# Kernel optimization log

Measured on AMD Instinct MI355X. Metric: run time of the kernel, lower is better.

Reference implementation:

```python
import jax, jax.numpy as jnp
import numpy as np
import math

B, S, DM = 2, 2048, 2048
NH, NKV, HD = 16, 4, 128
DFF = 8192
K_KEEP = DFF // 2  # sparsity_ratio = 0.5
EPS = 1e-6


def setup_inputs() -> dict:
    key = jax.random.key(0)
    ks = jax.random.split(key, 10)
    sc = 0.02
    return {
        "hidden_states": jax.random.normal(ks[0], (B, S, DM), dtype=jnp.float32),
        "wq": jax.random.normal(ks[1], (NH * HD, DM), dtype=jnp.float32) * sc,
        "wk": jax.random.normal(ks[2], (NKV * HD, DM), dtype=jnp.float32) * sc,
        "wv": jax.random.normal(ks[3], (NKV * HD, DM), dtype=jnp.float32) * sc,
        "wo": jax.random.normal(ks[4], (DM, NH * HD), dtype=jnp.float32) * sc,
        "ln1_w": jnp.ones((DM,), dtype=jnp.float32),
        "ln2_w": jnp.ones((DM,), dtype=jnp.float32),
        "w_gate": jax.random.normal(ks[5], (DFF, DM), dtype=jnp.float32) * sc,
        "w_up": jax.random.normal(ks[6], (DFF, DM), dtype=jnp.float32) * sc,
        "w_down": jax.random.normal(ks[7], (DM, DFF), dtype=jnp.float32) * sc,
    }


def _rmsnorm(x, w):
    var = jnp.mean(x * x, axis=-1, keepdims=True)
    return x * jax.lax.rsqrt(var + EPS) * w


def reference(hidden_states, wq, wk, wv, wo, ln1_w, ln2_w, w_gate, w_up, w_down):
    b, s, _ = hidden_states.shape
    # --- attention sub-block: RMSNorm -> GQA causal attention -> residual ---
    x = _rmsnorm(hidden_states, ln1_w)
    q = (x @ wq.T).reshape(b, s, NH, HD)
    k = (x @ wk.T).reshape(b, s, NKV, HD)
    v = (x @ wv.T).reshape(b, s, NKV, HD)
    # expand KV heads to match query heads (GQA)
    rep = NH // NKV
    k = jnp.repeat(k, rep, axis=2)
    v = jnp.repeat(v, rep, axis=2)
    scores = jnp.einsum('bqhd,bkhd->bhqk', q, k) / math.sqrt(HD)
    causal = jnp.tril(jnp.ones((s, s), dtype=bool))
    scores = jnp.where(causal, scores, jnp.finfo(scores.dtype).min)
    attn = jax.nn.softmax(scores, axis=-1)
    o = jnp.einsum('bhqk,bkhd->bqhd', attn, v).reshape(b, s, NH * HD)
    h = hidden_states + o @ wo.T
    # --- FFN sub-block: RMSNorm -> TopK-sparse SwiGLU -> residual ---
    y = _rmsnorm(h, ln2_w)
    gate = jax.nn.silu(y @ w_gate.T)  # [b, s, DFF]
    mag = jnp.abs(gate)
    thr = jax.lax.top_k(mag, K_KEEP)[0][..., -1:]  # kth-largest magnitude
    gate = jnp.where(mag >= thr, gate, 0.0)
    ff = (gate * (y @ w_up.T)) @ w_down.T
    return h + ff
```

## Files before the change

kernel.cpp:

```cpp
#include <hip/hip_runtime.h>
#include <stdint.h>

constexpr int SEQ    = 2048;
constexpr int DMODEL = 2048;
constexpr int NHEADS = 16;
constexpr int NKVH   = 4;
constexpr int HDIM   = 128;
constexpr int DFFN   = 8192;
constexpr int BATCH  = 2;
constexpr int MTOK   = BATCH * SEQ;
constexpr int KKEEP  = DFFN / 2;

typedef __bf16 bf16x8 __attribute__((ext_vector_type(8)));
typedef float  f32x4  __attribute__((ext_vector_type(4)));
typedef float  f32x16 __attribute__((ext_vector_type(16)));
typedef unsigned short u16;
typedef unsigned int   u32;

__device__ __forceinline__ u16 f2bu(float f) {
  u32 x = __builtin_bit_cast(u32, f);
  return (u16)((x + 0x7FFFu + ((x >> 16) & 1u)) >> 16);
}
__device__ __forceinline__ float b2f(u16 u) {
  u32 v = ((u32)u) << 16;
  return __builtin_bit_cast(float, v);
}
__device__ __forceinline__ void gl_lds16(const void* g, void* l) {
  __builtin_amdgcn_global_load_lds((const __attribute__((address_space(1))) u32*)g,
                                   (__attribute__((address_space(3))) u32*)l, 16, 0, 0);
}

__global__ __launch_bounds__(256) void cvt_kernel(const float* __restrict__ in,
                                                  u16* __restrict__ out, int n) {
  int i = (blockIdx.x * 256 + threadIdx.x) * 4;
  if (i >= n) return;
  float4 v = *(const float4*)(in + i);
  uint2 pk;
  pk.x = (u32)f2bu(v.x) | ((u32)f2bu(v.y) << 16);
  pk.y = (u32)f2bu(v.z) | ((u32)f2bu(v.w) << 16);
  *(uint2*)(out + i) = pk;
}

__global__ __launch_bounds__(256) void rmsnorm_kernel(const float* __restrict__ in,
                                                      const float* __restrict__ w,
                                                      u16* __restrict__ out) {
  const int tid = threadIdx.x;
  const size_t row = blockIdx.x;
  const float* x = in + row * DMODEL;
  float4 v0 = *(const float4*)(x + tid * 4);
  float4 v1 = *(const float4*)(x + 1024 + tid * 4);
  float s = v0.x*v0.x + v0.y*v0.y + v0.z*v0.z + v0.w*v0.w
          + v1.x*v1.x + v1.y*v1.y + v1.z*v1.z + v1.w*v1.w;
#pragma unroll
  for (int off = 1; off < 64; off <<= 1) s += __shfl_xor(s, off, 64);
  __shared__ float wsum[4];
  if ((tid & 63) == 0) wsum[tid >> 6] = s;
  __syncthreads();
  s = wsum[0] + wsum[1] + wsum[2] + wsum[3];
  const float rinv = rsqrtf(s * (1.0f / DMODEL) + 1e-6f);
  u16* o = out + row * DMODEL;
#pragma unroll
  for (int part = 0; part < 2; ++part) {
    int c = part * 1024 + tid * 4;
    float4 vv = (part == 0) ? v0 : v1;
    float4 wv = *(const float4*)(w + c);
    uint2 pk;
    pk.x = (u32)f2bu(vv.x * rinv * wv.x) | ((u32)f2bu(vv.y * rinv * wv.y) << 16);
    pk.y = (u32)f2bu(vv.z * rinv * wv.z) | ((u32)f2bu(vv.w * rinv * wv.w) << 16);
    *(uint2*)(o + c) = pk;
  }
}

template <int EPI>
__global__ __launch_bounds__(256, 2)
void gemm_bt(const u16* __restrict__ A, const u16* __restrict__ B,
             void* __restrict__ C, const float* res,
             int M, int N, int K) {
  __shared__ u16 As[2][128 * 64];
  __shared__ u16 Bs[2][128 * 64];
  const int tid = threadIdx.x;
  const int wave = tid >> 6, lane = tid & 63;
  const int nwg = gridDim.x * gridDim.y;
  const int lin = blockIdx.y * gridDim.x + blockIdx.x;
  const int swz = (lin & 7) * (nwg >> 3) + (lin >> 3);
  const int m0 = (swz / gridDim.x) * 128, n0 = (swz % gridDim.x) * 128;
  const int r_in = lane >> 3, chk = lane & 7;
  const int fk = lane >> 4, fc = lane & 15;
  const int wm = (wave >> 1) * 64, wn = (wave & 1) * 64;
  const int nt = K >> 6;
  f32x4 acc[4][4] = {};

  auto stage = [&](int buf, int t) {
    const int kt = t * 64;
#pragma unroll
    for (int i = 0; i < 4; ++i) {
      int row = wave * 32 + i * 8 + r_in;
      int gc = chk ^ (row & 7);
      gl_lds16(A + (size_t)(m0 + row) * K + kt + gc * 8, &As[buf][(wave * 32 + i * 8) * 64]);
    }
#pragma unroll
    for (int i = 0; i < 4; ++i) {
      int row = wave * 32 + i * 8 + r_in;
      int gc = chk ^ (row & 7);
      gl_lds16(B + (size_t)(n0 + row) * K + kt + gc * 8, &Bs[buf][(wave * 32 + i * 8) * 64]);
    }
  };

  stage(0, 0);
  asm volatile("s_waitcnt vmcnt(0)" ::: "memory");
  __builtin_amdgcn_s_barrier();

  for (int t = 0; t < nt; ++t) {
    if (t + 1 < nt) stage((t + 1) & 1, t + 1);
    const u16* Ab = As[t & 1];
    const u16* Bb = Bs[t & 1];
#pragma unroll
    for (int kk = 0; kk < 2; ++kk) {
      bf16x8 a[4], b[4];
#pragma unroll
      for (int i = 0; i < 4; ++i) {
        int row = wm + i * 16 + fc;
        int c = (kk * 4 + fk) ^ (row & 7);
        a[i] = *(const bf16x8*)(Ab + row * 64 + c * 8);
      }
#pragma unroll
      for (int j = 0; j < 4; ++j) {
        int row = wn + j * 16 + fc;
        int c = (kk * 4 + fk) ^ (row & 7);
        b[j] = *(const bf16x8*)(Bb + row * 64 + c * 8);
      }
#pragma unroll
      for (int i = 0; i < 4; ++i)
#pragma unroll
        for (int j = 0; j < 4; ++j)
          acc[i][j] = __builtin_amdgcn_mfma_f32_16x16x32_bf16(a[i], b[j], acc[i][j], 0, 0, 0);
    }
    asm volatile("s_waitcnt vmcnt(0)" ::: "memory");
    __builtin_amdgcn_s_barrier();
  }

  const int rb = fk * 4;
#pragma unroll
  for (int i = 0; i < 4; ++i) {
#pragma unroll
    for (int j = 0; j < 4; ++j) {
      int row = m0 + wm + i * 16 + rb;
      int col = n0 + wn + j * 16 + fc;
      f32x4 v = acc[i][j];
      if constexpr (EPI == 0) {
        u16* o = (u16*)C;
#pragma unroll
        for (int r = 0; r < 4; ++r) o[(size_t)(row + r) * N + col] = f2bu(v[r]);
      } else if constexpr (EPI == 1) {
        u16* o = (u16*)C;
        int bb = row >> 11, s = row & (SEQ - 1);
        int kvh = col >> 7, d = col & (HDIM - 1);
        size_t base = (((size_t)bb * NKVH + kvh) * HDIM + d) * SEQ + s;
        uint2 pk;
        pk.x = (u32)f2bu(v[0]) | ((u32)f2bu(v[1]) << 16);
        pk.y = (u32)f2bu(v[2]) | ((u32)f2bu(v[3]) << 16);
        *(uint2*)(o + base) = pk;
      } else if constexpr (EPI == 2) {
        float* o = (float*)C;
#pragma unroll
        for (int r = 0; r < 4; ++r) {
          size_t idx = (size_t)(row + r) * N + col;
          float rv = res[idx];
          o[idx] = v[r] + rv;
        }
      } else {
        float* o = (float*)C;
#pragma unroll
        for (int r = 0; r < 4; ++r) {
          float g = v[r];
          o[(size_t)(row + r) * N + col] = g / (1.0f + __expf(-g));
        }
      }
    }
  }
}

template <int EPI>
__global__ __launch_bounds__(512, 2)
void gemm256(const u16* __restrict__ A, const u16* __restrict__ B,
             void* __restrict__ C, int M, int N, int K) {
  __shared__ u16 As[2][2][128 * 64];
  __shared__ u16 Bs[2][2][128 * 64];
  const int tid = threadIdx.x;
  const int wave = tid >> 6, lane = tid & 63;
  const int nwg = gridDim.x * gridDim.y;
  const int lin = blockIdx.y * gridDim.x + blockIdx.x;
  const int swz = (lin & 7) * (nwg >> 3) + (lin >> 3);
  const int m0 = (swz / gridDim.x) * 256, n0 = (swz % gridDim.x) * 256;
  const int wm = wave >> 2, wn = wave & 3;
  const int fk = lane >> 4, fc = lane & 15;
  const int nt = K >> 6, ni = nt >> 1;
  const int s_sub = lane >> 3;
  const int s_gc  = (lane & 7) ^ s_sub;
  f32x4 acc[8][4] = {};
  bf16x8 b0[4], b1[4], a[4];

  auto sA = [&](int buf, int h, int t) {
    const u16* src = A + (size_t)(m0 + h * 128) * K + t * 64;
    u16* dst = &As[buf][h][0];
#pragma unroll
    for (int I = 0; I < 2; ++I) {
      int row = I * 64 + wave * 8 + s_sub;
      gl_lds16(src + (size_t)row * K + s_gc * 8, dst + (I * 512 + wave * 64) * 8);
    }
  };
  auto sB = [&](int buf, int h, int t) {
    const u16* src = B + (size_t)(n0 + h * 128) * K + t * 64;
    u16* dst = &Bs[buf][h][0];
#pragma unroll
    for (int I = 0; I < 2; ++I) {
      int row = I * 64 + wave * 8 + s_sub;
      gl_lds16(src + (size_t)row * K + s_gc * 8, dst + (I * 512 + wave * 64) * 8);
    }
  };
  auto rb = [&](const u16* Bh) {
#pragma unroll
    for (int n = 0; n < 4; ++n) {
      int row = (wn & 1) * 64 + n * 16 + fc;
      b0[n] = *(const bf16x8*)(Bh + row * 64 + ((fk) ^ (row & 7)) * 8);
      b1[n] = *(const bf16x8*)(Bh + row * 64 + ((4 + fk) ^ (row & 7)) * 8);
    }
  };
  auto ra = [&](const u16* Ah, int mh, int kk) {
#pragma unroll
    for (int m = 0; m < 4; ++m) {
      int row = mh * 64 + m * 16 + fc;
      a[m] = *(const bf16x8*)(Ah + row * 64 + ((kk * 4 + fk) ^ (row & 7)) * 8);
    }
  };
  auto midbar = [&]() {
    __builtin_amdgcn_s_barrier();
    asm volatile("s_waitcnt lgkmcnt(0)" ::: "memory");
    __builtin_amdgcn_sched_barrier(0);
    __builtin_amdgcn_s_setprio(1);
  };
  auto endbar = [&]() {
    __builtin_amdgcn_s_setprio(0);
    __builtin_amdgcn_s_barrier();
  };
  auto mfma16 = [&](int mh, bf16x8* bb) {
#pragma unroll
    for (int m = 0; m < 4; ++m)
#pragma unroll
      for (int n = 0; n < 4; ++n)
        acc[mh * 4 + m][n] =
            __builtin_amdgcn_mfma_f32_16x16x32_bf16(a[m], bb[n], acc[mh * 4 + m][n], 0, 0, 0);
  };

  sB(0, 0, 0); sB(0, 1, 0);
  sA(0, 0, 0); sA(0, 1, 0);
  sB(1, 0, 1); sB(1, 1, 1);
  asm volatile("s_waitcnt vmcnt(4)" ::: "memory");
  __builtin_amdgcn_s_barrier();

  for (int i = 0; i < ni; ++i) {
    const int u = 2 * i, v = 2 * i + 1;
    const bool more = (i + 1 < ni);
    const u16* Au = &As[0][wm][0];
    const u16* Bu = &Bs[0][wn >> 1][0];
    const u16* Av = &As[1][wm][0];
    const u16* Bv = &Bs[1][wn >> 1][0];
    rb(Bu); ra(Au, 0, 0); sA(1, 0, v);
    midbar(); mfma16(0, b0); endbar();
    ra(Au, 1, 0); sA(1, 1, v);
    midbar(); mfma16(1, b0); endbar();
    ra(Au, 0, 1); if (more) sB(0, 0, u + 2);
    midbar(); mfma16(0, b1); endbar();
    ra(Au, 1, 1); if (more) sB(0, 1, u + 2);
    midbar(); mfma16(1, b1);
    __builtin_amdgcn_s_setprio(0);
    if (more) asm volatile("s_waitcnt vmcnt(4)" ::: "memory");
    else      asm volatile("s_waitcnt vmcnt(0)" ::: "memory");
    __builtin_amdgcn_s_barrier();
    rb(Bv); ra(Av, 0, 0); if (more) sA(0, 0, u + 2);
    midbar(); mfma16(0, b0); endbar();
    ra(Av, 1, 0); if (more) sA(0, 1, u + 2);
    midbar(); mfma16(1, b0); endbar();
    ra(Av, 0, 1); if (more) sB(1, 0, v + 2);
    midbar(); mfma16(0, b1); endbar();
    ra(Av, 1, 1); if (more) sB(1, 1, v + 2);
    midbar(); mfma16(1, b1);
    __builtin_amdgcn_s_setprio(0);
    if (more) {
      asm volatile("s_waitcnt vmcnt(4)" ::: "memory");
    }
    __builtin_amdgcn_s_barrier();
  }

  const int rbase = fk * 4;
#pragma unroll
  for (int m = 0; m < 8; ++m) {
#pragma unroll
    for (int n = 0; n < 4; ++n) {
      int row = m0 + wm * 128 + m * 16 + rbase;
      int col = n0 + wn * 64 + n * 16 + fc;
      f32x4 vv = acc[m][n];
      if constexpr (EPI == 0) {
        u16* o = (u16*)C;
#pragma unroll
        for (int r = 0; r < 4; ++r) o[(size_t)(row + r) * N + col] = f2bu(vv[r]);
      } else {
        float* o = (float*)C;
#pragma unroll
        for (int r = 0; r < 4; ++r) {
          float g = vv[r];
          o[(size_t)(row + r) * N + col] = g / (1.0f + __expf(-g));
        }
      }
    }
  }
}

__global__ __launch_bounds__(256, 2)
void attn_kernel(const u16* __restrict__ Q, const u16* __restrict__ Kb,
                 const u16* __restrict__ Vt, u16* __restrict__ O) {
  __shared__ u16 Ksh[2 * 32 * 128];
  __shared__ u16 Vsh[2 * 128 * 32];
  const int tid = threadIdx.x, wave = tid >> 6, lane = tid & 63;
  const int half = lane >> 5, l31 = lane & 31;
  const int d_lin = blockIdx.x + gridDim.x * (blockIdx.y + gridDim.y * blockIdx.z);
  const int x = d_lin & 255, hi = d_lin >> 8;
  const int e = (x & 7) * 32 + (x >> 3);
  const int q = e & 7, h = (e >> 3) & 15, b = e >> 7;
  const int bx = hi ? 15 - q : q;
  const int kvh = h >> 2;
  const int qw = bx * 128 + wave * 32;
  const float SC = 0.08838834764831845f;
  const int ntb = bx * 4 + 4;
  const int nmy = bx * 4 + wave;

  bf16x8 qf[8];
  {
    const u16* qp = Q + ((size_t)(b * SEQ + qw + l31)) * DMODEL + h * HDIM + half * 8;
#pragma unroll
    for (int s = 0; s < 8; ++s) qf[s] = *(const bf16x8*)(qp + s * 16);
  }
  f32x16 oacc[4] = {};
  float m_run = -1e30f, l_run = 0.0f;
  const size_t vbase = ((size_t)(b * NKVH + kvh)) * HDIM * SEQ;
  const u16* kbase = Kb + (size_t)b * SEQ * (NKVH * HDIM) + kvh * HDIM;

  auto stage = [&](int bi, int k0) {
    u16* Kd = Ksh + bi * 4096;
    u16* Vd = Vsh + bi * 4096;
#pragma unroll
    for (int ii = 0; ii < 2; ++ii) {
      int inst = wave * 2 + ii;
      {
        int row = inst * 4 + (lane >> 4);
        int c = (lane & 15) ^ (row & 15);
        gl_lds16(kbase + (size_t)(k0 + row) * (NKVH * HDIM) + c * 8, Kd + inst * 512);
      }
      {
        int row = inst * 16 + (lane >> 2);
        int c = (lane & 3) ^ ((row >> 1) & 3);
        gl_lds16(Vt + vbase + (size_t)row * SEQ + k0 + c * 8, Vd + inst * 512);
      }
    }
  };

  stage(0, 0);
  __syncthreads();

  for (int t = 0; t < ntb; ++t) {
    if (t + 1 < ntb) stage((t + 1) & 1, (t + 1) * 32);
    if (t <= nmy) {
      const u16* Kd = Ksh + (t & 1) * 4096;
      const u16* Vd = Vsh + (t & 1) * 4096;
      f32x16 st = {};
#pragma unroll
      for (int s = 0; s < 8; ++s) {
        int c = (half + 2 * s) ^ (l31 & 15);
        bf16x8 kf = *(const bf16x8*)(Kd + l31 * 128 + c * 8);
        st = __builtin_amdgcn_mfma_f32_32x32x16_bf16(kf, qf[s], st, 0, 0, 0);
      }
      const bool diag = (t * 32 == qw);
      float sv[16];
#pragma unroll
      for (int r = 0; r < 16; ++r) {
        float xx = st[r] * SC;
        if (diag) {
          int kvl = (r & 3) + 8 * (r >> 2) + 4 * half;
          if (kvl > l31) xx = -1e30f;
        }
        sv[r] = xx;
      }
      float mx = sv[0];
#pragma unroll
      for (int r = 1; r < 16; ++r) mx = fmaxf(mx, sv[r]);
      mx = fmaxf(mx, __shfl_xor(mx, 32, 64));
      if (__any(mx > m_run + 4.0f)) {
        float mnew = fmaxf(m_run, mx);
        float alpha = __expf(m_run - mnew);
        m_run = mnew;
        l_run *= alpha;
#pragma unroll
        for (int r = 0; r < 16; ++r) {
          float ar = __shfl(alpha, (r & 3) + 8 * (r >> 2) + 4 * half, 64);
#pragma unroll
          for (int dt = 0; dt < 4; ++dt) oacc[dt][r] *= ar;
        }
      }
      float p[16];
      float rs = 0.0f;
#pragma unroll
      for (int r = 0; r < 16; ++r) { p[r] = __expf(sv[r] - m_run); rs += p[r]; }
      rs += __shfl_xor(rs, 32, 64);
      l_run += rs;
      u32 c01 = (u32)f2bu(p[0])  | ((u32)f2bu(p[1])  << 16);
      u32 c23 = (u32)f2bu(p[2])  | ((u32)f2bu(p[3])  << 16);
      u32 c45 = (u32)f2bu(p[4])  | ((u32)f2bu(p[5])  << 16);
      u32 c67 = (u32)f2bu(p[6])  | ((u32)f2bu(p[7])  << 16);
      u32 c89 = (u32)f2bu(p[8])  | ((u32)f2bu(p[9])  << 16);
      u32 cAB = (u32)f2bu(p[10]) | ((u32)f2bu(p[11]) << 16);
      u32 cCD = (u32)f2bu(p[12]) | ((u32)f2bu(p[13]) << 16);
      u32 cEF = (u32)f2bu(p[14]) | ((u32)f2bu(p[15]) << 16);
      u32 paw[2][4];
      {
        u32 sA = __shfl_xor(c01, 32, 64), sB = __shfl_xor(c23, 32, 64);
        u32 sC = __shfl_xor(c45, 32, 64), sD = __shfl_xor(c67, 32, 64);
        paw[0][0] = half ? sC : c01;  paw[0][1] = half ? sD : c23;
        paw[0][2] = half ? c45 : sA;  paw[0][3] = half ? c67 : sB;
      }
      {
        u32 sA = __shfl_xor(c89, 32, 64), sB = __shfl_xor(cAB, 32, 64);
        u32 sC = __shfl_xor(cCD, 32, 64), sD = __shfl_xor(cEF, 32, 64);
        paw[1][0] = half ? sC : c89;  paw[1][1] = half ? sD : cAB;
        paw[1][2] = half ? cCD : sA;  paw[1][3] = half ? cEF : sB;
      }
#pragma unroll
      for (int ks = 0; ks < 2; ++ks) {
        bf16x8 paf = __builtin_bit_cast(bf16x8, *(uint4*)&paw[ks][0]);
#pragma unroll
        for (int dt = 0; dt < 4; ++dt) {
          int row = dt * 32 + l31;
          int c = (half + 2 * ks) ^ ((row >> 1) & 3);
          bf16x8 vf = *(const bf16x8*)(Vd + row * 32 + c * 8);
          oacc[dt] = __builtin_amdgcn_mfma_f32_32x32x16_bf16(paf, vf, oacc[dt], 0, 0, 0);
        }
      }
    }
    __syncthreads();
  }

  float rinv = 1.0f / l_run;
  u16* ob = O + ((size_t)(b * SEQ + qw)) * DMODEL + h * HDIM + l31;
#pragma unroll
  for (int r = 0; r < 16; ++r) {
    int qr = (r & 3) + 8 * (r >> 2) + 4 * half;
    float ir = __shfl(rinv, qr, 64);
#pragma unroll
    for (int dt = 0; dt < 4; ++dt)
      ob[(size_t)qr * DMODEL + dt * 32] = f2bu(oacc[dt][r] * ir);
  }
}

__global__ __launch_bounds__(256)
void topk_kernel(const float* __restrict__ gate, u16* __restrict__ upact) {
  __shared__ u32 sabs[DFFN];
  __shared__ u32 hist[4][256];
  __shared__ u32 ss[257];
  __shared__ u32 sh_prefix, sh_rem;
  const int tid = threadIdx.x, wave = tid >> 6;
  const size_t row = blockIdx.x;
  const float* g = gate + row * DFFN;
  for (int it = 0; it < 4; ++it) {
    int e = it * 2048 + tid * 8;
    float4 a = *(const float4*)(g + e);
    float4 b = *(const float4*)(g + e + 4);
    sabs[e + 0] = __builtin_bit_cast(u32, a.x);
    sabs[e + 1] = __builtin_bit_cast(u32, a.y);
    sabs[e + 2] = __builtin_bit_cast(u32, a.z);
    sabs[e + 3] = __builtin_bit_cast(u32, a.w);
    sabs[e + 4] = __builtin_bit_cast(u32, b.x);
    sabs[e + 5] = __builtin_bit_cast(u32, b.y);
    sabs[e + 6] = __builtin_bit_cast(u32, b.z);
    sabs[e + 7] = __builtin_bit_cast(u32, b.w);
  }
  if (tid == 0) { sh_prefix = 0; sh_rem = KKEEP; }
  __syncthreads();
  for (int pass = 0; pass < 4; ++pass) {
    const int p = 24 - pass * 8;
    const u32 mask_hi = (pass == 0) ? 0u : (0xFFFFFFFFu << (p + 8));
    for (int i = tid; i < 1024; i += 256) ((u32*)hist)[i] = 0;
    __syncthreads();
    const u32 prefix = sh_prefix, rem = sh_rem;
    for (int it = 0; it < 4; ++it) {
      int e = it * 2048 + tid * 8;
#pragma unroll
      for (int j = 0; j < 8; ++j) {
        u32 mg = sabs[e + j] & 0x7FFFFFFFu;
        if ((mg & mask_hi) == (prefix & mask_hi))
          atomicAdd(&hist[wave][(mg >> p) & 0xFF], 1u);
      }
    }
    __syncthreads();
    ss[tid] = hist[0][tid] + hist[1][tid] + hist[2][tid] + hist[3][tid];
    if (tid == 0) ss[256] = 0;
    __syncthreads();
    for (int off = 1; off < 256; off <<= 1) {
      u32 v = (tid + off < 256) ? ss[tid + off] : 0u;
      __syncthreads();
      ss[tid] += v;
      __syncthreads();
    }
    if (ss[tid] >= rem && ss[tid + 1] < rem) {
      sh_prefix = prefix | ((u32)tid << p);
      sh_rem = rem - ss[tid + 1];
    }
    __syncthreads();
  }
  const u32 thr = sh_prefix;
  u16* ua = upact + row * DFFN;
  for (int it = 0; it < 4; ++it) {
    int e = it * 2048 + tid * 8;
    uint4 uv = *(const uint4*)(ua + e);
    const u16* up16 = (const u16*)&uv;
    u16 outp[8];
#pragma unroll
    for (int j = 0; j < 8; ++j) {
      u32 bits = sabs[e + j];
      u32 mg = bits & 0x7FFFFFFFu;
      float gg = __builtin_bit_cast(float, bits);
      float prod = (mg >= thr) ? gg * b2f(up16[j]) : 0.0f;
      outp[j] = f2bu(prod);
    }
    uint4 ov;
    ov.x = (u32)outp[0] | ((u32)outp[1] << 16);
    ov.y = (u32)outp[2] | ((u32)outp[3] << 16);
    ov.z = (u32)outp[4] | ((u32)outp[5] << 16);
    ov.w = (u32)outp[6] | ((u32)outp[7] << 16);
    *(uint4*)(ua + e) = ov;
  }
}

extern "C" void kernel_launch(void* const* d_in, const int* in_sizes, int n_in,
                              void* d_out, int out_size, void* d_ws, size_t ws_size,
                              hipStream_t stream) {
  const float* hidden = (const float*)d_in[0];
  const float* wq = (const float*)d_in[1];
  const float* wk = (const float*)d_in[2];
  const float* wv = (const float*)d_in[3];
  const float* wo = (const float*)d_in[4];
  const float* ln1 = (const float*)d_in[5];
  const float* ln2 = (const float*)d_in[6];
  const float* wg = (const float*)d_in[7];
  const float* wu = (const float*)d_in[8];
  const float* wd = (const float*)d_in[9];
  float* out = (float*)d_out;
  (void)in_sizes; (void)n_in; (void)out_size;

  size_t off = 0;
  auto alloc = [&](size_t n) { char* r = (char*)d_ws + off; off += (n + 255) & ~(size_t)255; return r; };
  u16* wq_b = (u16*)alloc((size_t)DMODEL * DMODEL * 2);
  u16* wk_b = (u16*)alloc((size_t)NKVH * HDIM * DMODEL * 2);
  u16* wv_b = (u16*)alloc((size_t)NKVH * HDIM * DMODEL * 2);
  u16* wo_b = (u16*)alloc((size_t)DMODEL * DMODEL * 2);
  u16* wg_b = (u16*)alloc((size_t)DFFN * DMODEL * 2);
  u16* tok  = (u16*)alloc((size_t)MTOK * DMODEL * 2);
  u16* upb  = (u16*)alloc((size_t)MTOK * DFFN * 2);
  char* S   = alloc((size_t)(MTOK / 2) * DFFN * 4);
  u16* qb   = (u16*)S;
  u16* kb   = (u16*)(S + (size_t)MTOK * DMODEL * 2);
  u16* vtb  = (u16*)(S + (size_t)MTOK * DMODEL * 2 + (size_t)MTOK * NKVH * HDIM * 2);
  u16* wu_b = (u16*)(S + (size_t)MTOK * DMODEL * 2 + 2 * (size_t)MTOK * NKVH * HDIM * 2);
  float* gateh = (float*)S;
  u16* wd_b = (u16*)S;
  const size_t needed = off;
  if (ws_size < needed) return;

  auto cvt = [&](const float* src, u16* dst, size_t n) {
    cvt_kernel<<<dim3((unsigned)(n / 1024)), 256, 0, stream>>>(src, dst, (int)n);
  };
  cvt(wq, wq_b, (size_t)DMODEL * DMODEL);
  cvt(wk, wk_b, (size_t)NKVH * HDIM * DMODEL);
  cvt(wv, wv_b, (size_t)NKVH * HDIM * DMODEL);
  cvt(wo, wo_b, (size_t)DMODEL * DMODEL);
  cvt(wg, wg_b, (size_t)DFFN * DMODEL);
  cvt(wu, wu_b, (size_t)DFFN * DMODEL);

  rmsnorm_kernel<<<MTOK, 256, 0, stream>>>(hidden, ln1, tok);

  gemm_bt<0><<<dim3(DMODEL / 128, MTOK / 128), 256, 0, stream>>>(
      tok, wq_b, qb, nullptr, MTOK, DMODEL, DMODEL);
  gemm_bt<0><<<dim3(NKVH * HDIM / 128, MTOK / 128), 256, 0, stream>>>(
      tok, wk_b, kb, nullptr, MTOK, NKVH * HDIM, DMODEL);
  gemm_bt<1><<<dim3(NKVH * HDIM / 128, MTOK / 128), 256, 0, stream>>>(
      tok, wv_b, vtb, nullptr, MTOK, NKVH * HDIM, DMODEL);

  attn_kernel<<<dim3(SEQ / 128, NHEADS, BATCH), 256, 0, stream>>>(qb, kb, vtb, tok);

  gemm_bt<2><<<dim3(DMODEL / 128, MTOK / 128), 256, 0, stream>>>(
      tok, wo_b, out, hidden, MTOK, DMODEL, DMODEL);

  rmsnorm_kernel<<<MTOK, 256, 0, stream>>>(out, ln2, tok);

  gemm256<0><<<dim3(DFFN / 256, MTOK / 256), 512, 0, stream>>>(
      tok, wu_b, upb, MTOK, DFFN, DMODEL);

  for (int half = 0; half < 2; ++half) {
    const u16* yh = tok + (size_t)half * (MTOK / 2) * DMODEL;
    u16* uph = upb + (size_t)half * (MTOK / 2) * DFFN;
    gemm256<3><<<dim3(DFFN / 256, (MTOK / 2) / 256), 512, 0, stream>>>(
        yh, wg_b, gateh, MTOK / 2, DFFN, DMODEL);
    topk_kernel<<<MTOK / 2, 256, 0, stream>>>(gateh, uph);
  }

  cvt(wd, wd_b, (size_t)DMODEL * DFFN);

  gemm_bt<2><<<dim3(DMODEL / 128, MTOK / 128), 256, 0, stream>>>(
      upb, wd_b, out, out, MTOK, DMODEL, DFFN);
}
```

Baseline: 986.2 us.

## Run down projection on 256-tile GEMM with split-K and a reduction kernel

```diff
diff --git a/kernel.cpp b/kernel.cpp
--- a/kernel.cpp
+++ b/kernel.cpp
@@ -39,6 +39,17 @@
   pk.x = (u32)f2bu(v.x) | ((u32)f2bu(v.y) << 16);
   pk.y = (u32)f2bu(v.z) | ((u32)f2bu(v.w) << 16);
   *(uint2*)(out + i) = pk;
+}
+
+__global__ __launch_bounds__(256) void redadd_kernel(float* __restrict__ out,
+                                                     const float* __restrict__ p0,
+                                                     const float* __restrict__ p1) {
+  int i = (blockIdx.x * 256 + threadIdx.x) * 4;
+  float4 o = *(const float4*)(out + i);
+  float4 a = *(const float4*)(p0 + i);
+  float4 b = *(const float4*)(p1 + i);
+  o.x += a.x + b.x; o.y += a.y + b.y; o.z += a.z + b.z; o.w += a.w + b.w;
+  *(float4*)(out + i) = o;
 }
 
 __global__ __launch_bounds__(256) void rmsnorm_kernel(const float* __restrict__ in,
@@ -183,7 +194,8 @@
 template <int EPI>
 __global__ __launch_bounds__(512, 2)
 void gemm256(const u16* __restrict__ A, const u16* __restrict__ B,
-             void* __restrict__ C, int M, int N, int K) {
+             void* __restrict__ C, void* __restrict__ C2,
+             int M, int N, int K, int lda) {
   __shared__ u16 As[2][2][128 * 64];
   __shared__ u16 Bs[2][2][128 * 64];
   const int tid = threadIdx.x;
@@ -192,6 +204,9 @@
   const int lin = blockIdx.y * gridDim.x + blockIdx.x;
   const int swz = (lin & 7) * (nwg >> 3) + (lin >> 3);
   const int m0 = (swz / gridDim.x) * 256, n0 = (swz % gridDim.x) * 256;
+  const int kh = blockIdx.z;
+  A += (size_t)kh * K;
+  B += (size_t)kh * K;
   const int wm = wave >> 2, wn = wave & 3;
   const int fk = lane >> 4, fc = lane & 15;
   const int nt = K >> 6, ni = nt >> 1;
@@ -201,21 +216,21 @@
   bf16x8 b0[4], b1[4], a[4];
 
   auto sA = [&](int buf, int h, int t) {
-    const u16* src = A + (size_t)(m0 + h * 128) * K + t * 64;
+    const u16* src = A + (size_t)(m0 + h * 128) * lda + t * 64;
     u16* dst = &As[buf][h][0];
 #pragma unroll
     for (int I = 0; I < 2; ++I) {
       int row = I * 64 + wave * 8 + s_sub;
-      gl_lds16(src + (size_t)row * K + s_gc * 8, dst + (I * 512 + wave * 64) * 8);
+      gl_lds16(src + (size_t)row * lda + s_gc * 8, dst + (I * 512 + wave * 64) * 8);
     }
   };
   auto sB = [&](int buf, int h, int t) {
-    const u16* src = B + (size_t)(n0 + h * 128) * K + t * 64;
+    const u16* src = B + (size_t)(n0 + h * 128) * lda + t * 64;
     u16* dst = &Bs[buf][h][0];
 #pragma unroll
     for (int I = 0; I < 2; ++I) {
       int row = I * 64 + wave * 8 + s_sub;
-      gl_lds16(src + (size_t)row * K + s_gc * 8, dst + (I * 512 + wave * 64) * 8);
+      gl_lds16(src + (size_t)row * lda + s_gc * 8, dst + (I * 512 + wave * 64) * 8);
     }
   };
   auto rb = [&](const u16* Bh) {
@@ -304,13 +319,17 @@
         u16* o = (u16*)C;
 #pragma unroll
         for (int r = 0; r < 4; ++r) o[(size_t)(row + r) * N + col] = f2bu(vv[r]);
-      } else {
+      } else if constexpr (EPI == 3) {
         float* o = (float*)C;
 #pragma unroll
         for (int r = 0; r < 4; ++r) {
           float g = vv[r];
           o[(size_t)(row + r) * N + col] = g / (1.0f + __expf(-g));
         }
+      } else {
+        float* o = (kh == 0) ? (float*)C : (float*)C2;
+#pragma unroll
+        for (int r = 0; r < 4; ++r) o[(size_t)(row + r) * N + col] = vv[r];
       }
     }
   }
@@ -571,6 +590,8 @@
   u16* wu_b = (u16*)(S + (size_t)MTOK * DMODEL * 2 + 2 * (size_t)MTOK * NKVH * HDIM * 2);
   float* gateh = (float*)S;
   u16* wd_b = (u16*)S;
+  float* p1 = (float*)(S + (size_t)32 * 1024 * 1024);
+  float* p0 = (float*)wg_b;
   const size_t needed = off;
   if (ws_size < needed) return;
 
@@ -601,18 +622,20 @@
   rmsnorm_kernel<<<MTOK, 256, 0, stream>>>(out, ln2, tok);
 
   gemm256<0><<<dim3(DFFN / 256, MTOK / 256), 512, 0, stream>>>(
-      tok, wu_b, upb, MTOK, DFFN, DMODEL);
+      tok, wu_b, upb, nullptr, MTOK, DFFN, DMODEL, DMODEL);
 
   for (int half = 0; half < 2; ++half) {
     const u16* yh = tok + (size_t)half * (MTOK / 2) * DMODEL;
     u16* uph = upb + (size_t)half * (MTOK / 2) * DFFN;
     gemm256<3><<<dim3(DFFN / 256, (MTOK / 2) / 256), 512, 0, stream>>>(
-        yh, wg_b, gateh, MTOK / 2, DFFN, DMODEL);
+        yh, wg_b, gateh, nullptr, MTOK / 2, DFFN, DMODEL, DMODEL);
     topk_kernel<<<MTOK / 2, 256, 0, stream>>>(gateh, uph);
   }
 
   cvt(wd, wd_b, (size_t)DMODEL * DFFN);
 
-  gemm_bt<2><<<dim3(DMODEL / 128, MTOK / 128), 256, 0, stream>>>(
-      upb, wd_b, out, out, MTOK, DMODEL, DFFN);
-}
+  gemm256<4><<<dim3(DMODEL / 256, MTOK / 256, 2), 512, 0, stream>>>(
+      upb, wd_b, p0, p1, MTOK, DMODEL, DFFN / 2, DFFN);
+
+  redadd_kernel<<<(MTOK * DMODEL) / 1024, 256, 0, stream>>>(out, p0, p1);
+}
```

Measured after the change: 969.8 us. About the same (-1.7%).
